# Kernel optimization log

Measured on AMD Instinct MI355X. Metric: run time of the kernel, lower is better.

The kernel has to match this reference:

```python
import jax, jax.numpy as jnp
import numpy as np

N, E, D = 100000, 400000, 128
LN_EPS = 1e-5
BN_EPS = 1e-5


def layer_norm(v, g, b):
    mu = jnp.mean(v, axis=-1, keepdims=True)
    var = jnp.var(v, axis=-1, keepdims=True)
    return (v - mu) * jax.lax.rsqrt(var + LN_EPS) * g + b


def setup_inputs() -> dict:
    key = jax.random.key(0)
    ks = jax.random.split(key, 12)
    s1 = 1.0 / np.sqrt(2 * D)
    s2 = 1.0 / np.sqrt(D)
    return {
        "x": jax.random.normal(ks[0], (N, D), jnp.float32),
        "edge_attr": jax.random.normal(ks[1], (E, D), jnp.float32),
        "W1": jax.random.uniform(ks[2], (2 * D, D), jnp.float32, -s1, s1),
        "b1": jax.random.uniform(ks[3], (D,), jnp.float32, -s1, s1),
        "g1": jnp.ones((D,), jnp.float32),
        "be1": jnp.zeros((D,), jnp.float32),
        "W2": jax.random.uniform(ks[4], (D, D), jnp.float32, -s2, s2),
        "b2": jax.random.uniform(ks[5], (D,), jnp.float32, -s2, s2),
        "g2": jnp.ones((D,), jnp.float32),
        "be2": jnp.zeros((D,), jnp.float32),
        "W3": jax.random.uniform(ks[6], (D, D), jnp.float32, -s2, s2),
        "b3": jax.random.uniform(ks[7], (D,), jnp.float32, -s2, s2),
        "eps": jnp.zeros((1,), jnp.float32),
        "bn_g": jnp.ones((D,), jnp.float32),
        "bn_b": jnp.zeros((D,), jnp.float32),
        "edge_index": jax.random.randint(ks[8], (2, E), 0, N, jnp.int64),
    }


def reference(x, edge_attr, W1, b1, g1, be1, W2, b2, g2, be2, W3, b3, eps, bn_g, bn_b, edge_index):
    row, col = edge_index[0], edge_index[1]
    identity_outer = x  # in_dim == out_dim -> projections are identity
    # GIN layer
    x_j = x[row]  # [E, D] gather
    xc = jnp.concatenate([x_j, edge_attr], axis=1)  # [E, 2D]
    h = jax.nn.relu(layer_norm(xc @ W1 + b1, g1, be1))  # edge_node_mlp
    agg = jax.ops.segment_sum(h, col, num_segments=x.shape[0])  # scatter_add over col
    out = (1.0 + eps) * x + agg
    out = jax.nn.relu(layer_norm(out @ W2 + b2, g2, be2)) @ W3 + b3  # mlp
    out = out + x  # inner residual (projection is None)
    out = out + identity_outer  # outer residual
    # BatchNorm1d (training mode: batch statistics, biased var)
    mu = jnp.mean(out, axis=0)
    var = jnp.var(out, axis=0)
    out = (out - mu) * jax.lax.rsqrt(var + BN_EPS) * bn_g + bn_b
    return out
```

## Files before the change

### kernel.cpp

```cpp
#include <hip/hip_runtime.h>

#define NN 100000
#define EE 400000

typedef unsigned short u16;
typedef unsigned int u32;
typedef short short8 __attribute__((ext_vector_type(8)));
typedef __bf16 bf16x8 __attribute__((ext_vector_type(8)));
typedef float f32x4 __attribute__((ext_vector_type(4)));

__device__ __forceinline__ short8 pack_bf16x8(f32x4 lo, f32x4 hi) {
  bf16x8 r;
#pragma unroll
  for (int j = 0; j < 4; ++j) { r[j] = (__bf16)lo[j]; r[4 + j] = (__bf16)hi[j]; }
  return __builtin_bit_cast(short8, r);
}

__device__ __forceinline__ u16 f2bf(float f) {
  return __builtin_bit_cast(unsigned short, (__bf16)f);
}

__device__ __forceinline__ float bf2f(short s) {
  u32 b = ((u32)(unsigned short)s) << 16;
  return __builtin_bit_cast(float, b);
}

__global__ void __launch_bounds__(256) k_cast(
    const float* __restrict__ x, u16* __restrict__ xb)
{
  const long total = (long)NN * 16;
  for (long i = (long)blockIdx.x * 256 + threadIdx.x; i < total;
       i += (long)gridDim.x * 256) {
    f32x4 v0 = reinterpret_cast<const f32x4*>(x)[i * 2];
    f32x4 v1 = reinterpret_cast<const f32x4*>(x)[i * 2 + 1];
    reinterpret_cast<short8*>(xb)[i] = pack_bf16x8(v0, v1);
  }
}

__global__ void __launch_bounds__(256) k_hist(
    const int* __restrict__ eidx, int* __restrict__ deg)
{
  for (int e = blockIdx.x * 256 + threadIdx.x; e < EE; e += gridDim.x * 256)
    atomicAdd(&deg[eidx[EE + e]], 1);
}

__global__ void __launch_bounds__(256) k_bsum(
    const int* __restrict__ deg, int* __restrict__ bsum)
{
  const int t = threadIdx.x;
  int idx = blockIdx.x * 1024 + t * 4;
  int s = 0;
#pragma unroll
  for (int i = 0; i < 4; ++i) if (idx + i < NN) s += deg[idx + i];
#pragma unroll
  for (int m = 1; m < 64; m <<= 1) s += __shfl_xor(s, m);
  __shared__ int ws_[4];
  if ((t & 63) == 0) ws_[t >> 6] = s;
  __syncthreads();
  if (t == 0) bsum[blockIdx.x] = ws_[0] + ws_[1] + ws_[2] + ws_[3];
}

__global__ void k_scanb(int* __restrict__ bsum, int* __restrict__ start)
{
  if (threadIdx.x == 0 && blockIdx.x == 0) {
    int run = 0;
    for (int b = 0; b < 98; ++b) { int t = bsum[b]; bsum[b] = run; run += t; }
    start[NN] = EE;
  }
}

__global__ void __launch_bounds__(256) k_scanc(
    const int* __restrict__ deg, const int* __restrict__ bsum,
    int* __restrict__ start, int* __restrict__ cur)
{
  const int t = threadIdx.x, lane = t & 63, wv = t >> 6;
  int idx = blockIdx.x * 1024 + t * 4;
  int c[4], ts = 0;
#pragma unroll
  for (int i = 0; i < 4; ++i) { c[i] = (idx + i < NN) ? deg[idx + i] : 0; ts += c[i]; }
  int incl = ts;
#pragma unroll
  for (int d = 1; d < 64; d <<= 1) {
    int u = __shfl_up(incl, d);
    if (lane >= d) incl += u;
  }
  __shared__ int wsum[4];
  if (lane == 63) wsum[wv] = incl;
  __syncthreads();
  int base = bsum[blockIdx.x];
  for (int w = 0; w < wv; ++w) base += wsum[w];
  int run = base + incl - ts;
#pragma unroll
  for (int i = 0; i < 4; ++i) {
    if (idx + i < NN) { start[idx + i] = run; cur[idx + i] = run; }
    run += c[i];
  }
}

__global__ void __launch_bounds__(256) k_fill(
    const int* __restrict__ eidx, int* __restrict__ cur, int* __restrict__ sid)
{
  for (int e = blockIdx.x * 256 + threadIdx.x; e < EE; e += gridDim.x * 256) {
    int c = eidx[EE + e];
    int p = atomicAdd(&cur[c], 1);
    sid[p] = e;
  }
}

__global__ void __launch_bounds__(512) k_edge(
    const u16* __restrict__ xb, const float* __restrict__ ea,
    const float* __restrict__ W1, const float* __restrict__ b1,
    const float* __restrict__ g1, const float* __restrict__ be1,
    const int* __restrict__ eidx, const int* __restrict__ sid,
    u16* __restrict__ hbuf)
{
  extern __shared__ char smem[];
  const int tid = threadIdx.x;

#pragma unroll
  for (int i = 0; i < 8; ++i) {
    int f = i * 512 + tid;
    int lo_ = f & 15;
    int kb_ = (f >> 4) & 3;
    int kc_ = (f >> 6) & 7;
    int nt_ = f >> 9;
    int n = nt_ * 16 + lo_;
    int k0 = kc_ * 32 + kb_ * 8;
    bf16x8 p;
#pragma unroll
    for (int j = 0; j < 8; ++j) p[j] = (__bf16)W1[(k0 + j) * 128 + n];
    *reinterpret_cast<short8*>(smem + f * 16) = __builtin_bit_cast(short8, p);
  }

  const int lane = tid & 63;
  const int wv = tid >> 6;
  const int lo = lane & 15;
  const int kb = lane >> 4;
  char* tb = smem + 65536 + wv * 2048;

  float b1v[8], g1v[8], bev[8];
#pragma unroll
  for (int nt = 0; nt < 8; ++nt) {
    int c = nt * 16 + lo;
    b1v[nt] = b1[c]; g1v[nt] = g1[c]; bev[nt] = be1[c];
  }
  __syncthreads();

  for (int t = blockIdx.x; t < EE / 128; t += gridDim.x) {
    const int pbase = t * 128 + wv * 16;
    const int p = pbase + lo;
    const int e = sid[p];
    const int r = eidx[e];

    short8 a[8];
#pragma unroll
    for (int kc = 0; kc < 4; ++kc)
      a[kc] = *reinterpret_cast<const short8*>(xb + (long)r * 128 + kc * 32 + kb * 8);
#pragma unroll
    for (int kc = 4; kc < 8; ++kc) {
      const float* src = ea + (long)e * 128 + (kc - 4) * 32 + kb * 8;
      f32x4 v0 = __builtin_nontemporal_load(reinterpret_cast<const f32x4*>(src));
      f32x4 v1 = __builtin_nontemporal_load(reinterpret_cast<const f32x4*>(src) + 1);
      a[kc] = pack_bf16x8(v0, v1);
    }

    f32x4 acc[8];
#pragma unroll
    for (int nt = 0; nt < 8; ++nt) acc[nt] = (f32x4){0.f, 0.f, 0.f, 0.f};

#pragma unroll
    for (int nt = 0; nt < 8; ++nt)
#pragma unroll
      for (int kc = 0; kc < 8; ++kc) {
        short8 b = *reinterpret_cast<const short8*>(
            smem + nt * 8192 + kc * 1024 + lane * 16);
        acc[nt] = __builtin_amdgcn_mfma_f32_16x16x32_bf16(a[kc], b, acc[nt], 0, 0, 0);
      }

    float s[4] = {0.f, 0.f, 0.f, 0.f};
    float q[4] = {0.f, 0.f, 0.f, 0.f};
#pragma unroll
    for (int nt = 0; nt < 8; ++nt)
#pragma unroll
      for (int i = 0; i < 4; ++i) {
        float v = acc[nt][i] + b1v[nt];
        acc[nt][i] = v;
        s[i] += v; q[i] += v * v;
      }
#pragma unroll
    for (int m = 1; m < 16; m <<= 1)
#pragma unroll
      for (int i = 0; i < 4; ++i) {
        s[i] += __shfl_xor(s[i], m);
        q[i] += __shfl_xor(q[i], m);
      }
    float mu[4], rs[4];
#pragma unroll
    for (int i = 0; i < 4; ++i) {
      mu[i] = s[i] * (1.f / 128.f);
      float var = q[i] * (1.f / 128.f) - mu[i] * mu[i];
      rs[i] = rsqrtf(var + 1e-5f);
    }

    u32 pk[8][4];
#pragma unroll
    for (int nt = 0; nt < 8; ++nt)
#pragma unroll
      for (int i = 0; i < 4; ++i) {
        float v = fmaxf((acc[nt][i] - mu[i]) * rs[i] * g1v[nt] + bev[nt], 0.f);
        float vn = __shfl_xor(v, 1);
        pk[nt][i] = (u32)f2bf(v) | ((u32)f2bf(vn) << 16);
      }

#pragma unroll
    for (int h = 0; h < 2; ++h) {
      if (h) asm volatile("s_waitcnt lgkmcnt(0)" ::: "memory");
      if ((kb >> 1) == h && !(lo & 1)) {
        int rl = (kb & 1) * 4;
#pragma unroll
        for (int nt = 0; nt < 8; ++nt)
#pragma unroll
          for (int i = 0; i < 4; ++i)
            *reinterpret_cast<u32*>(tb + (rl + i) * 256 + (nt * 16 + lo) * 2) = pk[nt][i];
      }
#pragma unroll
      for (int s4 = 0; s4 < 2; ++s4) {
        short8 rv = *reinterpret_cast<const short8*>(
            tb + (s4 * 4 + (lane >> 4)) * 256 + (lane & 15) * 16);
        __builtin_nontemporal_store(rv,
            reinterpret_cast<short8*>(hbuf + ((long)pbase + h * 8 + s4 * 4 + (lane >> 4)) * 128
                                      + (lane & 15) * 8));
      }
    }
  }
}

__global__ void __launch_bounds__(256) k_node1(
    const float* __restrict__ x, const u16* __restrict__ hbuf,
    const int* __restrict__ start,
    const float* __restrict__ W2, const float* __restrict__ b2,
    const float* __restrict__ g2, const float* __restrict__ be2,
    const float* __restrict__ epsp, u16* __restrict__ t1)
{
  __shared__ char smem[32768];
  const int tid = threadIdx.x;
#pragma unroll
  for (int i = 0; i < 8; ++i) {
    int f = i * 256 + tid;
    int lo_ = f & 15;
    int kb_ = (f >> 4) & 3;
    int kc_ = (f >> 6) & 3;
    int nt_ = f >> 8;
    int n = nt_ * 16 + lo_;
    int k0 = kc_ * 32 + kb_ * 8;
    bf16x8 p;
#pragma unroll
    for (int j = 0; j < 8; ++j) p[j] = (__bf16)W2[(k0 + j) * 128 + n];
    *reinterpret_cast<short8*>(smem + f * 16) = __builtin_bit_cast(short8, p);
  }

  const int lane = tid & 63, wv = tid >> 6, lo = lane & 15, kb = lane >> 4;
  const float ope = 1.f + epsp[0];
  __syncthreads();

  const int row = blockIdx.x * 64 + wv * 16 + lo;
  const int rc = row < NN ? row : NN - 1;

  float uacc[4][8];
#pragma unroll
  for (int kc = 0; kc < 4; ++kc)
#pragma unroll
    for (int j = 0; j < 8; ++j) uacc[kc][j] = 0.f;

  const int p0 = start[rc], p1 = start[rc + 1];
  for (int p = p0; p < p1; ++p) {
    const u16* hr = hbuf + (long)p * 128 + kb * 8;
#pragma unroll
    for (int kc = 0; kc < 4; ++kc) {
      short8 hv = __builtin_nontemporal_load(
          reinterpret_cast<const short8*>(hr + kc * 32));
#pragma unroll
      for (int j = 0; j < 8; ++j) uacc[kc][j] += bf2f(hv[j]);
    }
  }

  short8 a[4];
#pragma unroll
  for (int kc = 0; kc < 4; ++kc) {
    const float* xp = x + (long)rc * 128 + kc * 32 + kb * 8;
    f32x4 x0 = *reinterpret_cast<const f32x4*>(xp);
    f32x4 x1 = *reinterpret_cast<const f32x4*>(xp + 4);
    f32x4 u0, u1;
#pragma unroll
    for (int j = 0; j < 4; ++j) {
      u0[j] = fmaf(x0[j], ope, uacc[kc][j]);
      u1[j] = fmaf(x1[j], ope, uacc[kc][4 + j]);
    }
    a[kc] = pack_bf16x8(u0, u1);
  }

  f32x4 acc[8];
#pragma unroll
  for (int nt = 0; nt < 8; ++nt) acc[nt] = (f32x4){0.f, 0.f, 0.f, 0.f};

#pragma unroll
  for (int nt = 0; nt < 8; ++nt)
#pragma unroll
    for (int kc = 0; kc < 4; ++kc) {
      short8 b = *reinterpret_cast<const short8*>(smem + nt * 4096 + kc * 1024 + lane * 16);
      acc[nt] = __builtin_amdgcn_mfma_f32_16x16x32_bf16(a[kc], b, acc[nt], 0, 0, 0);
    }

  float b2v[8], g2v[8], bev[8];
#pragma unroll
  for (int nt = 0; nt < 8; ++nt) {
    int c = nt * 16 + lo;
    b2v[nt] = b2[c]; g2v[nt] = g2[c]; bev[nt] = be2[c];
  }

  float s[4] = {0.f, 0.f, 0.f, 0.f};
  float q[4] = {0.f, 0.f, 0.f, 0.f};
#pragma unroll
  for (int nt = 0; nt < 8; ++nt)
#pragma unroll
    for (int i = 0; i < 4; ++i) {
      float v = acc[nt][i] + b2v[nt];
      acc[nt][i] = v;
      s[i] += v; q[i] += v * v;
    }
#pragma unroll
  for (int m = 1; m < 16; m <<= 1)
#pragma unroll
    for (int i = 0; i < 4; ++i) {
      s[i] += __shfl_xor(s[i], m);
      q[i] += __shfl_xor(q[i], m);
    }
  float mu[4], rs[4];
  int rows[4];
#pragma unroll
  for (int i = 0; i < 4; ++i) {
    mu[i] = s[i] * (1.f / 128.f);
    float var = q[i] * (1.f / 128.f) - mu[i] * mu[i];
    rs[i] = rsqrtf(var + 1e-5f);
    rows[i] = blockIdx.x * 64 + wv * 16 + kb * 4 + i;
  }
#pragma unroll
  for (int nt = 0; nt < 8; ++nt)
#pragma unroll
    for (int i = 0; i < 4; ++i) {
      float v = fmaxf((acc[nt][i] - mu[i]) * rs[i] * g2v[nt] + bev[nt], 0.f);
      float vn = __shfl_xor(v, 1);
      if (!(lo & 1) && rows[i] < NN) {
        u32 pk = (u32)f2bf(v) | ((u32)f2bf(vn) << 16);
        *reinterpret_cast<u32*>(t1 + (long)rows[i] * 128 + nt * 16 + lo) = pk;
      }
    }
}

__global__ void __launch_bounds__(256) k_node2(
    const u16* __restrict__ t1, const float* __restrict__ x,
    const float* __restrict__ W3, const float* __restrict__ b3,
    u16* __restrict__ tmp, float* __restrict__ part)
{
  __shared__ char smem[32768];
  const int tid = threadIdx.x;
#pragma unroll
  for (int i = 0; i < 8; ++i) {
    int f = i * 256 + tid;
    int lo_ = f & 15;
    int kb_ = (f >> 4) & 3;
    int kc_ = (f >> 6) & 3;
    int nt_ = f >> 8;
    int n = nt_ * 16 + lo_;
    int k0 = kc_ * 32 + kb_ * 8;
    bf16x8 p;
#pragma unroll
    for (int j = 0; j < 8; ++j) p[j] = (__bf16)W3[(k0 + j) * 128 + n];
    *reinterpret_cast<short8*>(smem + f * 16) = __builtin_bit_cast(short8, p);
  }
  __syncthreads();

  const int lane = tid & 63, wv = tid >> 6, lo = lane & 15, kb = lane >> 4;
  const long rb = (long)blockIdx.x * 128 + wv * 32;

  short8 a[2][4];
#pragma unroll
  for (int mt = 0; mt < 2; ++mt) {
    long row = rb + mt * 16 + lo;
    long rc = row < NN ? row : (NN - 1);
#pragma unroll
    for (int kc = 0; kc < 4; ++kc)
      a[mt][kc] = *reinterpret_cast<const short8*>(t1 + rc * 128 + kc * 32 + kb * 8);
  }

  f32x4 acc[2][8];
#pragma unroll
  for (int mt = 0; mt < 2; ++mt)
#pragma unroll
    for (int nt = 0; nt < 8; ++nt)
      acc[mt][nt] = (f32x4){0.f, 0.f, 0.f, 0.f};

#pragma unroll
  for (int nt = 0; nt < 8; ++nt)
#pragma unroll
    for (int kc = 0; kc < 4; ++kc) {
      short8 b = *reinterpret_cast<const short8*>(smem + nt * 4096 + kc * 1024 + lane * 16);
      acc[0][nt] = __builtin_amdgcn_mfma_f32_16x16x32_bf16(a[0][kc], b, acc[0][nt], 0, 0, 0);
      acc[1][nt] = __builtin_amdgcn_mfma_f32_16x16x32_bf16(a[1][kc], b, acc[1][nt], 0, 0, 0);
    }

  float b3v[8];
#pragma unroll
  for (int nt = 0; nt < 8; ++nt) b3v[nt] = b3[nt * 16 + lo];

  float sn[8] = {0.f, 0.f, 0.f, 0.f, 0.f, 0.f, 0.f, 0.f};
  float qn[8] = {0.f, 0.f, 0.f, 0.f, 0.f, 0.f, 0.f, 0.f};

#pragma unroll
  for (int mt = 0; mt < 2; ++mt) {
    long rows[4], rc[4];
    bool val[4];
#pragma unroll
    for (int i = 0; i < 4; ++i) {
      rows[i] = rb + mt * 16 + kb * 4 + i;
      val[i] = rows[i] < NN;
      rc[i] = val[i] ? rows[i] : (NN - 1);
    }
#pragma unroll
    for (int nt = 0; nt < 8; ++nt)
#pragma unroll
      for (int i = 0; i < 4; ++i) {
        float v = acc[mt][nt][i] + b3v[nt] + 2.f * x[rc[i] * 128 + nt * 16 + lo];
        if (val[i]) { sn[nt] += v; qn[nt] += v * v; }
        float vn = __shfl_xor(v, 1);
        if (!(lo & 1) && val[i]) {
          u32 pk = (u32)f2bf(v) | ((u32)f2bf(vn) << 16);
          *reinterpret_cast<u32*>(tmp + rows[i] * 128 + nt * 16 + lo) = pk;
        }
      }
  }
#pragma unroll
  for (int nt = 0; nt < 8; ++nt) {
    sn[nt] += __shfl_xor(sn[nt], 16); sn[nt] += __shfl_xor(sn[nt], 32);
    qn[nt] += __shfl_xor(qn[nt], 16); qn[nt] += __shfl_xor(qn[nt], 32);
  }
  if (lane < 16) {
    long pr = ((long)blockIdx.x * 4 + wv) * 256;
#pragma unroll
    for (int nt = 0; nt < 8; ++nt) {
      part[pr + nt * 16 + lane] = sn[nt];
      part[pr + 128 + nt * 16 + lane] = qn[nt];
    }
  }
}

__global__ void __launch_bounds__(256) k_stats(
    const float* __restrict__ part, const float* __restrict__ bng,
    const float* __restrict__ bnb, float* __restrict__ stats2)
{
  const int c = blockIdx.x;
  const int tid = threadIdx.x;
  float s = 0.f, q = 0.f;
  for (int i = tid; i < 3128; i += 256) {
    s += part[(long)i * 256 + c];
    q += part[(long)i * 256 + 128 + c];
  }
#pragma unroll
  for (int m = 1; m < 64; m <<= 1) { s += __shfl_xor(s, m); q += __shfl_xor(q, m); }
  __shared__ float rs_[4], rq_[4];
  const int wv = tid >> 6;
  if ((tid & 63) == 0) { rs_[wv] = s; rq_[wv] = q; }
  __syncthreads();
  if (tid == 0) {
    s = rs_[0] + rs_[1] + rs_[2] + rs_[3];
    q = rq_[0] + rq_[1] + rq_[2] + rq_[3];
    float mu = s * (1.f / (float)NN);
    float var = q * (1.f / (float)NN) - mu * mu;
    float sc = rsqrtf(var + 1e-5f) * bng[c];
    stats2[c] = sc;
    stats2[128 + c] = bnb[c] - mu * sc;
  }
}

__global__ void __launch_bounds__(256) k_apply(
    const u16* __restrict__ tmp, const float* __restrict__ stats2,
    float* __restrict__ out)
{
  const long total = (long)NN * 16;
  for (long i = (long)blockIdx.x * 256 + threadIdx.x; i < total;
       i += (long)gridDim.x * 256) {
    int db = (int)((i & 15) << 3);
    short8 hv = reinterpret_cast<const short8*>(tmp)[i];
    f32x4 sc0 = *reinterpret_cast<const f32x4*>(stats2 + db);
    f32x4 sc1 = *reinterpret_cast<const f32x4*>(stats2 + db + 4);
    f32x4 sh0 = *reinterpret_cast<const f32x4*>(stats2 + 128 + db);
    f32x4 sh1 = *reinterpret_cast<const f32x4*>(stats2 + 128 + db + 4);
    f32x4 o0, o1;
#pragma unroll
    for (int j = 0; j < 4; ++j) {
      o0[j] = fmaf(bf2f(hv[j]), sc0[j], sh0[j]);
      o1[j] = fmaf(bf2f(hv[4 + j]), sc1[j], sh1[j]);
    }
    reinterpret_cast<f32x4*>(out)[i * 2] = o0;
    reinterpret_cast<f32x4*>(out)[i * 2 + 1] = o1;
  }
}

extern "C" void kernel_launch(void* const* d_in, const int* in_sizes, int n_in,
                              void* d_out, int out_size, void* d_ws, size_t ws_size,
                              hipStream_t stream)
{
  const float* x   = (const float*)d_in[0];
  const float* ea  = (const float*)d_in[1];
  const float* W1  = (const float*)d_in[2];
  const float* b1  = (const float*)d_in[3];
  const float* g1  = (const float*)d_in[4];
  const float* be1 = (const float*)d_in[5];
  const float* W2  = (const float*)d_in[6];
  const float* b2  = (const float*)d_in[7];
  const float* g2  = (const float*)d_in[8];
  const float* be2 = (const float*)d_in[9];
  const float* W3  = (const float*)d_in[10];
  const float* b3  = (const float*)d_in[11];
  const float* eps = (const float*)d_in[12];
  const float* bng = (const float*)d_in[13];
  const float* bnb = (const float*)d_in[14];
  const int*   eidx = (const int*)d_in[15];
  float* out = (float*)d_out;

  u16*   hbuf   = (u16*)d_ws;
  u16*   t1     = (u16*)((char*)d_ws + 102400000L);
  u16*   xb     = t1;
  u16*   tmp    = (u16*)d_ws;
  float* part   = (float*)((char*)d_ws + 128000000L);
  float* stats2 = part + 3128L * 256;
  int*   deg    = (int*)(stats2 + 256);
  int*   start  = deg + NN;
  int*   cur    = start + NN + 1;
  int*   bsum   = cur + NN;
  int*   sid    = bsum + 128;

  (void)hipFuncSetAttribute(reinterpret_cast<const void*>(k_edge),
                            hipFuncAttributeMaxDynamicSharedMemorySize, 81920);

  hipMemsetAsync(deg, 0, (size_t)NN * 4, stream);
  k_cast  <<<1024, 256, 0, stream>>>(x, xb);
  k_hist  <<<512, 256, 0, stream>>>(eidx, deg);
  k_bsum  <<<98, 256, 0, stream>>>(deg, bsum);
  k_scanb <<<1, 64, 0, stream>>>(bsum, start);
  k_scanc <<<98, 256, 0, stream>>>(deg, bsum, start, cur);
  k_fill  <<<512, 256, 0, stream>>>(eidx, cur, sid);
  k_edge  <<<512, 512, 81920, stream>>>(xb, ea, W1, b1, g1, be1, eidx, sid, hbuf);
  k_node1 <<<(NN + 63) / 64, 256, 0, stream>>>(x, hbuf, start, W2, b2, g2, be2, eps, t1);
  k_node2 <<<(NN + 127) / 128, 256, 0, stream>>>(t1, x, W3, b3, tmp, part);
  k_stats <<<128, 256, 0, stream>>>(part, bng, bnb, stats2);
  k_apply <<<2048, 256, 0, stream>>>(tmp, stats2, out);
}
```

Before: 269.6 us.

## Prefetch edge tiles, sort nodes by degree, store source rows, use bf16 x

The edge kernel now double-buffers its A operands, loading the next tile's gathered features while the current tile's MFMAs run. The fill kernel stores the source row next to each sorted edge id, so one dependent gather is removed. New kernels bucket nodes by in-degree into a permutation, so each node1 wave handles rows of similar degree and divergence in the aggregation loop shrinks. node1 also unrolls the aggregation by two and reads bf16 x instead of fp32. In exchange there are three extra small launches, more workspace, and x is rounded to bf16 before the (1+eps)x term.

```diff
diff --git a/kernel.cpp b/kernel.cpp
--- a/kernel.cpp
+++ b/kernel.cpp
@@ -38,8 +38,9 @@
 }
 
 __global__ void __launch_bounds__(256) k_hist(
-    const int* __restrict__ eidx, int* __restrict__ deg)
-{
+    const int* __restrict__ eidx, int* __restrict__ deg, int* __restrict__ dcnt)
+{
+  if (blockIdx.x == 0 && threadIdx.x < 64) dcnt[threadIdx.x] = 0;
   for (int e = blockIdx.x * 256 + threadIdx.x; e < EE; e += gridDim.x * 256)
     atomicAdd(&deg[eidx[EE + e]], 1);
 }
@@ -98,24 +99,65 @@
 }
 
 __global__ void __launch_bounds__(256) k_fill(
-    const int* __restrict__ eidx, int* __restrict__ cur, int* __restrict__ sid)
+    const int* __restrict__ eidx, int* __restrict__ cur,
+    int* __restrict__ sid, int* __restrict__ srow)
 {
   for (int e = blockIdx.x * 256 + threadIdx.x; e < EE; e += gridDim.x * 256) {
     int c = eidx[EE + e];
     int p = atomicAdd(&cur[c], 1);
     sid[p] = e;
-  }
-}
-
-__global__ void __launch_bounds__(512) k_edge(
+    srow[p] = eidx[e];
+  }
+}
+
+__global__ void __launch_bounds__(256) k_dcount(
+    const int* __restrict__ deg, int* __restrict__ dcnt)
+{
+  __shared__ int lh[64];
+  if (threadIdx.x < 64) lh[threadIdx.x] = 0;
+  __syncthreads();
+  for (int n = blockIdx.x * 256 + threadIdx.x; n < NN; n += gridDim.x * 256) {
+    int b = deg[n]; b = b > 63 ? 63 : b;
+    atomicAdd(&lh[b], 1);
+  }
+  __syncthreads();
+  if (threadIdx.x < 64 && lh[threadIdx.x]) atomicAdd(&dcnt[threadIdx.x], lh[threadIdx.x]);
+}
+
+__global__ void k_dscan(const int* __restrict__ dcnt, int* __restrict__ dcur)
+{
+  int t = threadIdx.x;
+  int v = dcnt[t];
+  int incl = v;
+#pragma unroll
+  for (int d = 1; d < 64; d <<= 1) {
+    int u = __shfl_up(incl, d);
+    if (t >= d) incl += u;
+  }
+  dcur[t] = incl - v;
+}
+
+__global__ void __launch_bounds__(256) k_dfill(
+    const int* __restrict__ deg, int* __restrict__ dcur, int* __restrict__ perm)
+{
+  for (int n = blockIdx.x * 256 + threadIdx.x; n < NN; n += gridDim.x * 256) {
+    int b = deg[n]; b = b > 63 ? 63 : b;
+    int pos = atomicAdd(&dcur[b], 1);
+    perm[pos] = n;
+  }
+}
+
+__global__ void __launch_bounds__(512, 4) k_edge(
     const u16* __restrict__ xb, const float* __restrict__ ea,
     const float* __restrict__ W1, const float* __restrict__ b1,
     const float* __restrict__ g1, const float* __restrict__ be1,
-    const int* __restrict__ eidx, const int* __restrict__ sid,
+    const int* __restrict__ sid, const int* __restrict__ srow,
     u16* __restrict__ hbuf)
 {
   extern __shared__ char smem[];
   const int tid = threadIdx.x;
+  const int NT = EE / 128;
+  const int G = gridDim.x;
 
 #pragma unroll
   for (int i = 0; i < 8; ++i) {
@@ -146,36 +188,45 @@
   }
   __syncthreads();
 
-  for (int t = blockIdx.x; t < EE / 128; t += gridDim.x) {
-    const int pbase = t * 128 + wv * 16;
-    const int p = pbase + lo;
-    const int e = sid[p];
-    const int r = eidx[e];
-
-    short8 a[8];
+  short8 aA[8], aB[8];
+
+  auto loadA = [&](int e, int r, short8* A) {
 #pragma unroll
     for (int kc = 0; kc < 4; ++kc)
-      a[kc] = *reinterpret_cast<const short8*>(xb + (long)r * 128 + kc * 32 + kb * 8);
+      A[kc] = *reinterpret_cast<const short8*>(xb + (long)r * 128 + kc * 32 + kb * 8);
 #pragma unroll
     for (int kc = 4; kc < 8; ++kc) {
       const float* src = ea + (long)e * 128 + (kc - 4) * 32 + kb * 8;
       f32x4 v0 = __builtin_nontemporal_load(reinterpret_cast<const f32x4*>(src));
       f32x4 v1 = __builtin_nontemporal_load(reinterpret_cast<const f32x4*>(src) + 1);
-      a[kc] = pack_bf16x8(v0, v1);
+      A[kc] = pack_bf16x8(v0, v1);
+    }
+  };
+
+  auto process = [&](int t, short8* A, short8* B) {
+    const int pbase = t * 128 + wv * 16;
+    const int tn = t + G;
+    const bool pf = tn < NT;
+    int en = 0, rn = 0;
+    if (pf) {
+      int pn = tn * 128 + wv * 16 + lo;
+      en = sid[pn];
+      rn = srow[pn];
     }
 
     f32x4 acc[8];
 #pragma unroll
     for (int nt = 0; nt < 8; ++nt) acc[nt] = (f32x4){0.f, 0.f, 0.f, 0.f};
-
 #pragma unroll
     for (int nt = 0; nt < 8; ++nt)
 #pragma unroll
       for (int kc = 0; kc < 8; ++kc) {
         short8 b = *reinterpret_cast<const short8*>(
             smem + nt * 8192 + kc * 1024 + lane * 16);
-        acc[nt] = __builtin_amdgcn_mfma_f32_16x16x32_bf16(a[kc], b, acc[nt], 0, 0, 0);
+        acc[nt] = __builtin_amdgcn_mfma_f32_16x16x32_bf16(A[kc], b, acc[nt], 0, 0, 0);
       }
+
+    if (pf) loadA(en, rn, B);
 
     float s[4] = {0.f, 0.f, 0.f, 0.f};
     float q[4] = {0.f, 0.f, 0.f, 0.f};
@@ -202,27 +253,20 @@
       rs[i] = rsqrtf(var + 1e-5f);
     }
 
-    u32 pk[8][4];
-#pragma unroll
-    for (int nt = 0; nt < 8; ++nt)
-#pragma unroll
-      for (int i = 0; i < 4; ++i) {
-        float v = fmaxf((acc[nt][i] - mu[i]) * rs[i] * g1v[nt] + bev[nt], 0.f);
-        float vn = __shfl_xor(v, 1);
-        pk[nt][i] = (u32)f2bf(v) | ((u32)f2bf(vn) << 16);
-      }
-
 #pragma unroll
     for (int h = 0; h < 2; ++h) {
       if (h) asm volatile("s_waitcnt lgkmcnt(0)" ::: "memory");
-      if ((kb >> 1) == h && !(lo & 1)) {
-        int rl = (kb & 1) * 4;
-#pragma unroll
-        for (int nt = 0; nt < 8; ++nt)
-#pragma unroll
-          for (int i = 0; i < 4; ++i)
-            *reinterpret_cast<u32*>(tb + (rl + i) * 256 + (nt * 16 + lo) * 2) = pk[nt][i];
-      }
+#pragma unroll
+      for (int nt = 0; nt < 8; ++nt)
+#pragma unroll
+        for (int i = 0; i < 4; ++i) {
+          float v = fmaxf((acc[nt][i] - mu[i]) * rs[i] * g1v[nt] + bev[nt], 0.f);
+          float vn = __shfl_xor(v, 1);
+          if ((kb >> 1) == h && !(lo & 1)) {
+            *reinterpret_cast<u32*>(tb + ((kb & 1) * 4 + i) * 256 + (nt * 16 + lo) * 2)
+                = (u32)f2bf(v) | ((u32)f2bf(vn) << 16);
+          }
+        }
 #pragma unroll
       for (int s4 = 0; s4 < 2; ++s4) {
         short8 rv = *reinterpret_cast<const short8*>(
@@ -232,12 +276,26 @@
                                       + (lane & 15) * 8));
       }
     }
+  };
+
+  int t = blockIdx.x;
+  if (t < NT) {
+    int p0 = t * 128 + wv * 16 + lo;
+    loadA(sid[p0], srow[p0], aA);
+    for (;;) {
+      process(t, aA, aB);
+      t += G;
+      if (t >= NT) break;
+      process(t, aB, aA);
+      t += G;
+      if (t >= NT) break;
+    }
   }
 }
 
 __global__ void __launch_bounds__(256) k_node1(
-    const float* __restrict__ x, const u16* __restrict__ hbuf,
-    const int* __restrict__ start,
+    const u16* __restrict__ xb, const u16* __restrict__ hbuf,
+    const int* __restrict__ start, const int* __restrict__ perm,
     const float* __restrict__ W2, const float* __restrict__ b2,
     const float* __restrict__ g2, const float* __restrict__ be2,
     const float* __restrict__ epsp, u16* __restrict__ t1)
@@ -263,8 +321,8 @@
   const float ope = 1.f + epsp[0];
   __syncthreads();
 
-  const int row = blockIdx.x * 64 + wv * 16 + lo;
-  const int rc = row < NN ? row : NN - 1;
+  const int pidx = blockIdx.x * 64 + wv * 16 + lo;
+  const int n = perm[pidx < NN ? pidx : NN - 1];
 
   float uacc[4][8];
 #pragma unroll
@@ -272,13 +330,27 @@
 #pragma unroll
     for (int j = 0; j < 8; ++j) uacc[kc][j] = 0.f;
 
-  const int p0 = start[rc], p1 = start[rc + 1];
-  for (int p = p0; p < p1; ++p) {
-    const u16* hr = hbuf + (long)p * 128 + kb * 8;
+  const int p0 = start[n], p1 = start[n + 1];
+  int p = p0;
+  for (; p + 2 <= p1; p += 2) {
+    const u16* h0 = hbuf + (long)p * 128 + kb * 8;
+    short8 hv0[4], hv1[4];
 #pragma unroll
     for (int kc = 0; kc < 4; ++kc) {
-      short8 hv = __builtin_nontemporal_load(
-          reinterpret_cast<const short8*>(hr + kc * 32));
+      hv0[kc] = __builtin_nontemporal_load(reinterpret_cast<const short8*>(h0 + kc * 32));
+      hv1[kc] = __builtin_nontemporal_load(reinterpret_cast<const short8*>(h0 + 128 + kc * 32));
+    }
+#pragma unroll
+    for (int kc = 0; kc < 4; ++kc)
+#pragma unroll
+      for (int j = 0; j < 8; ++j)
+        uacc[kc][j] += bf2f(hv0[kc][j]) + bf2f(hv1[kc][j]);
+  }
+  if (p < p1) {
+    const u16* h0 = hbuf + (long)p * 128 + kb * 8;
+#pragma unroll
+    for (int kc = 0; kc < 4; ++kc) {
+      short8 hv = __builtin_nontemporal_load(reinterpret_cast<const short8*>(h0 + kc * 32));
 #pragma unroll
       for (int j = 0; j < 8; ++j) uacc[kc][j] += bf2f(hv[j]);
     }
@@ -287,14 +359,12 @@
   short8 a[4];
 #pragma unroll
   for (int kc = 0; kc < 4; ++kc) {
-    const float* xp = x + (long)rc * 128 + kc * 32 + kb * 8;
-    f32x4 x0 = *reinterpret_cast<const f32x4*>(xp);
-    f32x4 x1 = *reinterpret_cast<const f32x4*>(xp + 4);
+    short8 xv = *reinterpret_cast<const short8*>(xb + (long)n * 128 + kc * 32 + kb * 8);
     f32x4 u0, u1;
 #pragma unroll
     for (int j = 0; j < 4; ++j) {
-      u0[j] = fmaf(x0[j], ope, uacc[kc][j]);
-      u1[j] = fmaf(x1[j], ope, uacc[kc][4 + j]);
+      u0[j] = fmaf(bf2f(xv[j]), ope, uacc[kc][j]);
+      u1[j] = fmaf(bf2f(xv[4 + j]), ope, uacc[kc][4 + j]);
     }
     a[kc] = pack_bf16x8(u0, u1);
   }
@@ -336,13 +406,14 @@
       q[i] += __shfl_xor(q[i], m);
     }
   float mu[4], rs[4];
-  int rows[4];
+  int prow[4];
 #pragma unroll
   for (int i = 0; i < 4; ++i) {
     mu[i] = s[i] * (1.f / 128.f);
     float var = q[i] * (1.f / 128.f) - mu[i] * mu[i];
     rs[i] = rsqrtf(var + 1e-5f);
-    rows[i] = blockIdx.x * 64 + wv * 16 + kb * 4 + i;
+    int idx = blockIdx.x * 64 + wv * 16 + kb * 4 + i;
+    prow[i] = idx < NN ? perm[idx] : -1;
   }
 #pragma unroll
   for (int nt = 0; nt < 8; ++nt)
@@ -350,9 +421,9 @@
     for (int i = 0; i < 4; ++i) {
       float v = fmaxf((acc[nt][i] - mu[i]) * rs[i] * g2v[nt] + bev[nt], 0.f);
       float vn = __shfl_xor(v, 1);
-      if (!(lo & 1) && rows[i] < NN) {
+      if (!(lo & 1) && prow[i] >= 0) {
         u32 pk = (u32)f2bf(v) | ((u32)f2bf(vn) << 16);
-        *reinterpret_cast<u32*>(t1 + (long)rows[i] * 128 + nt * 16 + lo) = pk;
+        *reinterpret_cast<u32*>(t1 + (long)prow[i] * 128 + nt * 16 + lo) = pk;
       }
     }
 }
@@ -530,29 +601,36 @@
 
   u16*   hbuf   = (u16*)d_ws;
   u16*   t1     = (u16*)((char*)d_ws + 102400000L);
-  u16*   xb     = t1;
+  u16*   xb     = (u16*)((char*)d_ws + 128000000L);
   u16*   tmp    = (u16*)d_ws;
-  float* part   = (float*)((char*)d_ws + 128000000L);
+  float* part   = (float*)((char*)d_ws + 153600000L);
   float* stats2 = part + 3128L * 256;
   int*   deg    = (int*)(stats2 + 256);
   int*   start  = deg + NN;
   int*   cur    = start + NN + 1;
   int*   bsum   = cur + NN;
   int*   sid    = bsum + 128;
+  int*   srow   = sid + EE;
+  int*   perm   = srow + EE;
+  int*   dcnt   = perm + NN;
+  int*   dcur   = dcnt + 64;
 
   (void)hipFuncSetAttribute(reinterpret_cast<const void*>(k_edge),
                             hipFuncAttributeMaxDynamicSharedMemorySize, 81920);
 
   hipMemsetAsync(deg, 0, (size_t)NN * 4, stream);
-  k_cast  <<<1024, 256, 0, stream>>>(x, xb);
-  k_hist  <<<512, 256, 0, stream>>>(eidx, deg);
-  k_bsum  <<<98, 256, 0, stream>>>(deg, bsum);
-  k_scanb <<<1, 64, 0, stream>>>(bsum, start);
-  k_scanc <<<98, 256, 0, stream>>>(deg, bsum, start, cur);
-  k_fill  <<<512, 256, 0, stream>>>(eidx, cur, sid);
-  k_edge  <<<512, 512, 81920, stream>>>(xb, ea, W1, b1, g1, be1, eidx, sid, hbuf);
-  k_node1 <<<(NN + 63) / 64, 256, 0, stream>>>(x, hbuf, start, W2, b2, g2, be2, eps, t1);
-  k_node2 <<<(NN + 127) / 128, 256, 0, stream>>>(t1, x, W3, b3, tmp, part);
-  k_stats <<<128, 256, 0, stream>>>(part, bng, bnb, stats2);
-  k_apply <<<2048, 256, 0, stream>>>(tmp, stats2, out);
-}
+  k_cast   <<<1024, 256, 0, stream>>>(x, xb);
+  k_hist   <<<512, 256, 0, stream>>>(eidx, deg, dcnt);
+  k_bsum   <<<98, 256, 0, stream>>>(deg, bsum);
+  k_scanb  <<<1, 64, 0, stream>>>(bsum, start);
+  k_scanc  <<<98, 256, 0, stream>>>(deg, bsum, start, cur);
+  k_dcount <<<391, 256, 0, stream>>>(deg, dcnt);
+  k_dscan  <<<1, 64, 0, stream>>>(dcnt, dcur);
+  k_dfill  <<<391, 256, 0, stream>>>(deg, dcur, perm);
+  k_fill   <<<512, 256, 0, stream>>>(eidx, cur, sid, srow);
+  k_edge   <<<512, 512, 81920, stream>>>(xb, ea, W1, b1, g1, be1, sid, srow, hbuf);
+  k_node1  <<<(NN + 63) / 64, 256, 0, stream>>>(xb, hbuf, start, perm, W2, b2, g2, be2, eps, t1);
+  k_node2  <<<(NN + 127) / 128, 256, 0, stream>>>(t1, x, W3, b3, tmp, part);
+  k_stats  <<<128, 256, 0, stream>>>(part, bng, bnb, stats2);
+  k_apply  <<<2048, 256, 0, stream>>>(tmp, stats2, out);
+}
```

Result: slower. 799.5 us (+196.5%).
